# Kernel tuning notes

Measured on AMD Instinct MI355X. Metric: run time of the kernel, lower is better.

The kernel has to match this reference:

```python
import jax, jax.numpy as jnp
import numpy as np

B, N_Z, N_E, D = 16, 2048, 2048, 512

def setup_inputs() -> dict:
    key = jax.random.key(0)
    kz, ke, km = jax.random.split(key, 3)
    z = jax.random.normal(kz, (B, N_Z, D), dtype=jnp.float32)
    e = jax.random.normal(ke, (B, N_E, D), dtype=jnp.float32)
    M = jax.random.normal(km, (D, D), dtype=jnp.float32)  # init: normal(0, 1)
    return {"z": z, "e": e, "M": M}

def reference(z, e, M):
    # a = z @ M @ e^T : [B, Nz, Ne]
    zM = jnp.einsum('bnd,de->bne', z, M)
    a = jnp.einsum('bnd,bmd->bnm', zM, e)
    a = jax.nn.sigmoid(a)
    # softmax over dim=1 (the Nz axis), as in the torch code
    A = jax.nn.softmax(a, axis=1)
    # out = A @ e : [B, Nz, D]
    return jnp.einsum('bnm,bmd->bnd', A, e)
```

## Files before the change

### kernel.cpp

```cpp
#include <hip/hip_runtime.h>
#include <hip/hip_bf16.h>
#include <stdint.h>

#define BB 16
#define NZ 2048
#define NE 2048
#define DD 512

typedef unsigned short u16;
typedef __attribute__((ext_vector_type(8))) _Float16 f16x8;
typedef __attribute__((ext_vector_type(8))) short s16x8;
typedef __attribute__((ext_vector_type(4))) float f32x4;

__device__ __forceinline__ u16 f2h(float f) {
  _Float16 h = (_Float16)f;
  return __builtin_bit_cast(u16, h);
}

__device__ __forceinline__ float h2f(u16 h) {
  return (float)__builtin_bit_cast(_Float16, h);
}

__device__ __forceinline__ void gload_lds16(const void* g, void* l) {
  auto gp = (const __attribute__((address_space(1))) uint32_t*)g;
  auto lp = (__attribute__((address_space(3))) uint32_t*)l;
  __builtin_amdgcn_global_load_lds(gp, lp, 16, 0, 0);
}

#define FENCE() asm volatile("" ::: "memory")
#define BARRIER() do { FENCE(); __builtin_amdgcn_s_barrier(); FENCE(); } while (0)
#define WAIT_VM(n) asm volatile("s_waitcnt vmcnt(" #n ")" ::: "memory")

__global__ void k_cvt(const float* __restrict__ in, u16* __restrict__ out, int n8) {
  int i = blockIdx.x * blockDim.x + threadIdx.x;
  int stride = gridDim.x * blockDim.x;
  for (; i < n8; i += stride) {
    float4 v0 = ((const float4*)in)[i * 2];
    float4 v1 = ((const float4*)in)[i * 2 + 1];
    s16x8 o;
    o[0] = (short)f2h(v0.x); o[1] = (short)f2h(v0.y);
    o[2] = (short)f2h(v0.z); o[3] = (short)f2h(v0.w);
    o[4] = (short)f2h(v1.x); o[5] = (short)f2h(v1.y);
    o[6] = (short)f2h(v1.z); o[7] = (short)f2h(v1.w);
    ((s16x8*)out)[i] = o;
  }
}

__global__ void k_mt(const float* __restrict__ M, u16* __restrict__ Mt) {
  __shared__ float t[32][33];
  int bx = blockIdx.x * 32;
  int by = blockIdx.y * 32;
  for (int r = 0; r < 32; r += 8)
    t[threadIdx.y + r][threadIdx.x] = M[(size_t)(by + threadIdx.y + r) * DD + bx + threadIdx.x];
  __syncthreads();
  for (int r = 0; r < 32; r += 8)
    Mt[(size_t)(bx + threadIdx.y + r) * DD + by + threadIdx.x] = f2h(t[threadIdx.x][threadIdx.y + r]);
}

__global__ void k_et(const u16* __restrict__ eH, const float* __restrict__ cs,
                     u16* __restrict__ eT) {
  __shared__ u16 sm[64 * 72];
  const int t = threadIdx.x;
  const int b = blockIdx.z;
  const int d0 = blockIdx.x * 64;
  const int m0 = blockIdx.y * 64;
  const u16* eb = eH + (size_t)b * NE * DD;
  const float* csb = cs + (size_t)b * NE;
#pragma unroll
  for (int it = 0; it < 2; ++it) {
    int idx = it * 256 + t;
    int ml = idx >> 3;
    int dc = idx & 7;
    s16x8 v = *(const s16x8*)(eb + (size_t)(m0 + ml) * DD + d0 + dc * 8);
    float sc = 2048.0f / csb[m0 + ml];
    int bl = ml >> 3, il = ml & 7;
#pragma unroll
    for (int j = 0; j < 8; ++j) {
      int d = dc * 8 + j;
      int pc = ((bl ^ j) << 3) + il;
      sm[d * 72 + pc] = f2h(h2f((u16)v[j]) * sc);
    }
  }
  __syncthreads();
  u16* eTb = eT + (size_t)b * DD * NE;
#pragma unroll
  for (int it = 0; it < 2; ++it) {
    int idx = it * 256 + t;
    int dl = idx >> 3;
    int mc = idx & 7;
    int pb = mc ^ (dl & 7);
    s16x8 v = *(const s16x8*)&sm[dl * 72 + pb * 8];
    *(s16x8*)(eTb + (size_t)(d0 + dl) * NE + m0 + mc * 8) = v;
  }
}

template<int EPI, int KDIM>
__global__ __launch_bounds__(256, 3) void k_gemm(
    const u16* __restrict__ A, const u16* __restrict__ Bt, void* __restrict__ Cp,
    int Ndim, long long sAb, long long sBb, long long sCb,
    float* __restrict__ colsum, int csld)
{
  extern __shared__ char lds[];
  constexpr int NT = KDIM / 32;

  const int gx = gridDim.x, gy = gridDim.y;
  const int nwg = gx * gy * gridDim.z;
  const int hid = blockIdx.x + gx * (blockIdx.y + gy * blockIdx.z);
  const int logical = (hid & 7) * (nwg >> 3) + (hid >> 3);
  const int bx = logical % gx;
  const int rem0 = logical / gx;
  const int by = rem0 % gy;
  const int bz = rem0 / gy;

  const int tid = threadIdx.x;
  const int lane = tid & 63;
  const int wid = tid >> 6;
  const int wr = wid >> 1;
  const int wc = wid & 1;

  const int row0 = by * 128;
  const int col0 = bx * 128;

  const u16* Ab = A + (long long)bz * sAb;
  const u16* Bb = Bt + (long long)bz * sBb;

  const u16* srcA[2]; const u16* srcB[2];
#pragma unroll
  for (int c = 0; c < 2; ++c) {
    int idx = c * 256 + tid;
    int r = idx >> 2;
    int cL = idx & 3;
    int q = cL ^ ((r >> 1) & 3);
    srcA[c] = Ab + (long long)(row0 + r) * KDIM + q * 8;
    srcB[c] = Bb + (long long)(col0 + r) * KDIM + q * 8;
  }

  auto stage = [&](int t) {
    const int k0 = t * 32;
    char* d = lds + (t % 3) * 16384;
#pragma unroll
    for (int c = 0; c < 2; ++c)
      gload_lds16(srcA[c] + k0, d + (c * 256 + wid * 64) * 16);
#pragma unroll
    for (int c = 0; c < 2; ++c)
      gload_lds16(srcB[c] + k0, d + 8192 + (c * 256 + wid * 64) * 16);
  };

  const int p15 = lane & 15;
  const int cswz = (lane >> 4) ^ ((p15 >> 1) & 3);

  f32x4 acc[4][4] = {};

  stage(0);
  stage(1);
  WAIT_VM(4);
  BARRIER();

  for (int t = 0; t < NT; ++t) {
    char* lA = lds + (t % 3) * 16384;
    char* lB = lA + 8192;

    f16x8 af[4], bf[4];
#pragma unroll
    for (int m = 0; m < 4; ++m) {
      int r = wr * 64 + m * 16 + p15;
      int c4 = (lane >> 4) ^ ((r >> 1) & 3);
      af[m] = *(const f16x8*)(lA + r * 64 + c4 * 16);
    }
#pragma unroll
    for (int n = 0; n < 4; ++n) {
      int r = wc * 64 + n * 16 + p15;
      int c4 = (lane >> 4) ^ ((r >> 1) & 3);
      bf[n] = *(const f16x8*)(lB + r * 64 + c4 * 16);
    }
#pragma unroll
    for (int m = 0; m < 4; ++m)
#pragma unroll
      for (int n = 0; n < 4; ++n)
        acc[m][n] = __builtin_amdgcn_mfma_f32_16x16x32_f16(af[m], bf[n], acc[m][n], 0, 0, 0);

    BARRIER();
    if (t + 2 < NT) stage(t + 2);
    if (t + 1 < NT) {
      if (t + 2 < NT) { WAIT_VM(4); } else { WAIT_VM(0); }
      BARRIER();
    }
  }

  __syncthreads();

  const int rr = (lane >> 4) * 4;
  const int cc = lane & 15;
  const int grow = row0 + wr * 64;
  const int gcol = col0 + wc * 64;
  (void)cswz;

  if constexpr (EPI == 0 || EPI == 1) {
    char* wb = lds + wid * 8192;
    float csum[4] = {0.f, 0.f, 0.f, 0.f};
#pragma unroll
    for (int m = 0; m < 4; ++m)
#pragma unroll
      for (int n = 0; n < 4; ++n)
#pragma unroll
        for (int j = 0; j < 4; ++j) {
          float x = acc[m][n][j];
          float v;
          if constexpr (EPI == 1) {
            float s = 1.f / (1.f + __expf(-x));
            v = __expf(s);
            csum[n] += v;
          } else {
            v = x;
          }
          int rl = m * 16 + rr + j;
          int col = n * 16 + cc;
          int chunk = (col >> 3) ^ (rl & 7);
          *(u16*)(wb + rl * 128 + chunk * 16 + ((col * 2) & 15)) = f2h(v);
        }
    if constexpr (EPI == 1) {
#pragma unroll
      for (int n = 0; n < 4; ++n) {
        float v = csum[n];
        v += __shfl_xor(v, 16, 64);
        v += __shfl_xor(v, 32, 64);
        if ((lane >> 4) == 0)
          atomicAdd(&colsum[(long long)bz * csld + gcol + n * 16 + cc], v);
      }
    }
    __syncthreads();
    u16* C = (u16*)Cp + (long long)bz * sCb;
#pragma unroll
    for (int s = 0; s < 8; ++s) {
      int rl = (lane >> 3) + s * 8;
      int chunk = (lane & 7) ^ (rl & 7);
      f16x8 v = *(const f16x8*)(wb + rl * 128 + chunk * 16);
      *(f16x8*)(&C[(long long)(grow + rl) * Ndim + gcol + (lane & 7) * 8]) = v;
    }
  } else {
    float* C = (float*)Cp + (long long)bz * sCb;
    char* wb = lds + wid * 8192;
#pragma unroll
    for (int h = 0; h < 2; ++h) {
      if (h) __syncthreads();
#pragma unroll
      for (int mm = 0; mm < 2; ++mm) {
        int m = h * 2 + mm;
#pragma unroll
        for (int n = 0; n < 4; ++n)
#pragma unroll
          for (int j = 0; j < 4; ++j) {
            int rl = mm * 16 + rr + j;
            int col = n * 16 + cc;
            int chunk = (col >> 2) ^ (rl & 15);
            *(float*)(wb + rl * 256 + chunk * 16 + ((col * 4) & 15)) =
                acc[m][n][j] * (1.0f / 2048.0f);
          }
      }
      __syncthreads();
#pragma unroll
      for (int s = 0; s < 8; ++s) {
        int rl = (lane >> 4) + s * 4;
        int chunk = (lane & 15) ^ (rl & 15);
        f32x4 v = *(const f32x4*)(wb + rl * 256 + chunk * 16);
        *(f32x4*)(&C[(long long)(grow + h * 32 + rl) * Ndim + gcol + (lane & 15) * 4]) = v;
      }
    }
  }
}

extern "C" void kernel_launch(void* const* d_in, const int* in_sizes, int n_in,
                              void* d_out, int out_size, void* d_ws, size_t ws_size,
                              hipStream_t stream) {
  const float* z = (const float*)d_in[0];
  const float* e = (const float*)d_in[1];
  const float* M = (const float*)d_in[2];
  float* out = (float*)d_out;
  char* ws = (char*)d_ws;

  u16* S    = (u16*)(ws + 0LL);
  u16* zM   = (u16*)(ws + 134217728LL);
  u16* zH   = (u16*)(ws + 167772160LL);
  u16* eH   = (u16*)(ws + 201326592LL);
  u16* Mt   = (u16*)(ws + 234881024LL);
  float* cs = (float*)(ws + 235405312LL);

  hipMemsetAsync(cs, 0, (size_t)BB * NE * sizeof(float), stream);

  k_cvt<<<4096, 256, 0, stream>>>(z, zH, BB * NZ * DD / 8);
  k_cvt<<<4096, 256, 0, stream>>>(e, eH, BB * NE * DD / 8);
  k_mt<<<dim3(16, 16), dim3(32, 8), 0, stream>>>(M, Mt);

  k_gemm<0, 512><<<dim3(DD / 128, (BB * NZ) / 128, 1), 256, 49152, stream>>>(
      zH, Mt, zM, DD, 0LL, 0LL, 0LL, nullptr, 0);

  k_gemm<1, 512><<<dim3(NE / 128, NZ / 128, BB), 256, 49152, stream>>>(
      zM, eH, S, NE,
      (long long)NZ * DD, (long long)NE * DD, (long long)NZ * NE, cs, NE);

  u16* eT = zH;
  k_et<<<dim3(DD / 64, NE / 64, BB), 256, 0, stream>>>(eH, cs, eT);

  k_gemm<2, 2048><<<dim3(DD / 128, NZ / 128, BB), 256, 49152, stream>>>(
      S, eT, out, DD,
      (long long)NZ * NE, (long long)DD * NE, (long long)NZ * DD, nullptr, 0);
}
```

Measured before the change: 277.6 us.

## Use two-wave 128x128 GEMM tiles with larger per-wave tiles and double buffering

Reworks the GEMM kernel from 4 waves (each computing 64x64) to 2 waves per block, each computing a 128x64 sub-tile with 8x4 MFMA accumulators. The LDS pipeline drops from triple buffering to double buffering with a full vmcnt(0) wait each step, and LDS drops to 32KB. The aim is more fragment reuse per LDS load and lower per-block overhead. In exchange it doubles register pressure, halves the waves per block, and removes prefetch depth, so load latency is less well hidden.

```diff
diff --git a/kernel.cpp b/kernel.cpp
--- a/kernel.cpp
+++ b/kernel.cpp
@@ -29,6 +29,7 @@
 
 #define FENCE() asm volatile("" ::: "memory")
 #define BARRIER() do { FENCE(); __builtin_amdgcn_s_barrier(); FENCE(); } while (0)
+#define WAIT_LGKM0() asm volatile("s_waitcnt lgkmcnt(0)" ::: "memory")
 #define WAIT_VM(n) asm volatile("s_waitcnt vmcnt(" #n ")" ::: "memory")
 
 __global__ void k_cvt(const float* __restrict__ in, u16* __restrict__ out, int n8) {
@@ -95,7 +96,7 @@
 }
 
 template<int EPI, int KDIM>
-__global__ __launch_bounds__(256, 3) void k_gemm(
+__global__ __launch_bounds__(128, 2) void k_gemm(
     const u16* __restrict__ A, const u16* __restrict__ Bt, void* __restrict__ Cp,
     int Ndim, long long sAb, long long sBb, long long sCb,
     float* __restrict__ colsum, int csld)
@@ -115,8 +116,6 @@
   const int tid = threadIdx.x;
   const int lane = tid & 63;
   const int wid = tid >> 6;
-  const int wr = wid >> 1;
-  const int wc = wid & 1;
 
   const int row0 = by * 128;
   const int col0 = bx * 128;
@@ -124,82 +123,78 @@
   const u16* Ab = A + (long long)bz * sAb;
   const u16* Bb = Bt + (long long)bz * sBb;
 
-  const u16* srcA[2]; const u16* srcB[2];
-#pragma unroll
-  for (int c = 0; c < 2; ++c) {
-    int idx = c * 256 + tid;
+  const u16* pA[4]; const u16* pB[4];
+#pragma unroll
+  for (int c = 0; c < 4; ++c) {
+    int idx = c * 128 + tid;
     int r = idx >> 2;
     int cL = idx & 3;
     int q = cL ^ ((r >> 1) & 3);
-    srcA[c] = Ab + (long long)(row0 + r) * KDIM + q * 8;
-    srcB[c] = Bb + (long long)(col0 + r) * KDIM + q * 8;
-  }
-
-  auto stage = [&](int t) {
-    const int k0 = t * 32;
-    char* d = lds + (t % 3) * 16384;
-#pragma unroll
-    for (int c = 0; c < 2; ++c)
-      gload_lds16(srcA[c] + k0, d + (c * 256 + wid * 64) * 16);
-#pragma unroll
-    for (int c = 0; c < 2; ++c)
-      gload_lds16(srcB[c] + k0, d + 8192 + (c * 256 + wid * 64) * 16);
+    pA[c] = Ab + (long long)(row0 + r) * KDIM + q * 8;
+    pB[c] = Bb + (long long)(col0 + r) * KDIM + q * 8;
+  }
+
+  auto stage = [&](char* s) {
+#pragma unroll
+    for (int c = 0; c < 4; ++c) {
+      gload_lds16(pA[c], s + (c * 128 + wid * 64) * 16);
+      pA[c] += 32;
+    }
+#pragma unroll
+    for (int c = 0; c < 4; ++c) {
+      gload_lds16(pB[c], s + 8192 + (c * 128 + wid * 64) * 16);
+      pB[c] += 32;
+    }
   };
 
   const int p15 = lane & 15;
-  const int cswz = (lane >> 4) ^ ((p15 >> 1) & 3);
-
-  f32x4 acc[4][4] = {};
-
-  stage(0);
-  stage(1);
-  WAIT_VM(4);
+  const int c4 = (lane >> 4) ^ ((p15 >> 1) & 3);
+  const int laneA = p15 * 64 + c4 * 16;
+  const int laneB = 8192 + wid * 4096 + p15 * 64 + c4 * 16;
+
+  f32x4 acc[8][4] = {};
+
+  char* sl0 = lds;
+  char* sl1 = lds + 16384;
+
+  stage(sl0);
+  WAIT_VM(0);
   BARRIER();
 
   for (int t = 0; t < NT; ++t) {
-    char* lA = lds + (t % 3) * 16384;
-    char* lB = lA + 8192;
-
-    f16x8 af[4], bf[4];
-#pragma unroll
-    for (int m = 0; m < 4; ++m) {
-      int r = wr * 64 + m * 16 + p15;
-      int c4 = (lane >> 4) ^ ((r >> 1) & 3);
-      af[m] = *(const f16x8*)(lA + r * 64 + c4 * 16);
-    }
-#pragma unroll
-    for (int n = 0; n < 4; ++n) {
-      int r = wc * 64 + n * 16 + p15;
-      int c4 = (lane >> 4) ^ ((r >> 1) & 3);
-      bf[n] = *(const f16x8*)(lB + r * 64 + c4 * 16);
-    }
-#pragma unroll
-    for (int m = 0; m < 4; ++m)
+    f16x8 af[8], bf[4];
+#pragma unroll
+    for (int m = 0; m < 8; ++m) af[m] = *(const f16x8*)(sl0 + laneA + m * 1024);
+#pragma unroll
+    for (int n = 0; n < 4; ++n) bf[n] = *(const f16x8*)(sl0 + laneB + n * 1024);
+#pragma unroll
+    for (int m = 0; m < 8; ++m)
 #pragma unroll
       for (int n = 0; n < 4; ++n)
         acc[m][n] = __builtin_amdgcn_mfma_f32_16x16x32_f16(af[m], bf[n], acc[m][n], 0, 0, 0);
 
-    BARRIER();
-    if (t + 2 < NT) stage(t + 2);
     if (t + 1 < NT) {
-      if (t + 2 < NT) { WAIT_VM(4); } else { WAIT_VM(0); }
+      WAIT_LGKM0();
       BARRIER();
-    }
+      stage(sl1);
+      WAIT_VM(0);
+      BARRIER();
+    }
+    char* tmp = sl0; sl0 = sl1; sl1 = tmp;
   }
 
   __syncthreads();
 
   const int rr = (lane >> 4) * 4;
   const int cc = lane & 15;
-  const int grow = row0 + wr * 64;
-  const int gcol = col0 + wc * 64;
-  (void)cswz;
+  const int grow = row0;
+  const int gcol = col0 + wid * 64;
 
   if constexpr (EPI == 0 || EPI == 1) {
-    char* wb = lds + wid * 8192;
+    char* wb = lds + wid * 16384;
     float csum[4] = {0.f, 0.f, 0.f, 0.f};
 #pragma unroll
-    for (int m = 0; m < 4; ++m)
+    for (int m = 0; m < 8; ++m)
 #pragma unroll
       for (int n = 0; n < 4; ++n)
 #pragma unroll
@@ -231,7 +226,7 @@
     __syncthreads();
     u16* C = (u16*)Cp + (long long)bz * sCb;
 #pragma unroll
-    for (int s = 0; s < 8; ++s) {
+    for (int s = 0; s < 16; ++s) {
       int rl = (lane >> 3) + s * 8;
       int chunk = (lane & 7) ^ (rl & 7);
       f16x8 v = *(const f16x8*)(wb + rl * 128 + chunk * 16);
@@ -239,13 +234,13 @@
     }
   } else {
     float* C = (float*)Cp + (long long)bz * sCb;
-    char* wb = lds + wid * 8192;
+    char* wb = lds + wid * 16384;
 #pragma unroll
     for (int h = 0; h < 2; ++h) {
       if (h) __syncthreads();
 #pragma unroll
-      for (int mm = 0; mm < 2; ++mm) {
-        int m = h * 2 + mm;
+      for (int mm = 0; mm < 4; ++mm) {
+        int m = h * 4 + mm;
 #pragma unroll
         for (int n = 0; n < 4; ++n)
 #pragma unroll
@@ -259,11 +254,11 @@
       }
       __syncthreads();
 #pragma unroll
-      for (int s = 0; s < 8; ++s) {
+      for (int s = 0; s < 16; ++s) {
         int rl = (lane >> 4) + s * 4;
         int chunk = (lane & 15) ^ (rl & 15);
         f32x4 v = *(const f32x4*)(wb + rl * 256 + chunk * 16);
-        *(f32x4*)(&C[(long long)(grow + h * 32 + rl) * Ndim + gcol + (lane & 15) * 4]) = v;
+        *(f32x4*)(&C[(long long)(grow + h * 64 + rl) * Ndim + gcol + (lane & 15) * 4]) = v;
       }
     }
   }
@@ -291,17 +286,17 @@
   k_cvt<<<4096, 256, 0, stream>>>(e, eH, BB * NE * DD / 8);
   k_mt<<<dim3(16, 16), dim3(32, 8), 0, stream>>>(M, Mt);
 
-  k_gemm<0, 512><<<dim3(DD / 128, (BB * NZ) / 128, 1), 256, 49152, stream>>>(
+  k_gemm<0, 512><<<dim3(DD / 128, (BB * NZ) / 128, 1), 128, 32768, stream>>>(
       zH, Mt, zM, DD, 0LL, 0LL, 0LL, nullptr, 0);
 
-  k_gemm<1, 512><<<dim3(NE / 128, NZ / 128, BB), 256, 49152, stream>>>(
+  k_gemm<1, 512><<<dim3(NE / 128, NZ / 128, BB), 128, 32768, stream>>>(
       zM, eH, S, NE,
       (long long)NZ * DD, (long long)NE * DD, (long long)NZ * NE, cs, NE);
 
   u16* eT = zH;
   k_et<<<dim3(DD / 64, NE / 64, BB), 256, 0, stream>>>(eH, cs, eT);
 
-  k_gemm<2, 2048><<<dim3(DD / 128, NZ / 128, BB), 256, 49152, stream>>>(
+  k_gemm<2, 2048><<<dim3(DD / 128, NZ / 128, BB), 128, 32768, stream>>>(
       S, eT, out, DD,
       (long long)NZ * NE, (long long)DD * NE, (long long)NZ * DD, nullptr, 0);
 }
```

Result: slower. 286.9 us (+3.4%).
